# Performance work log

Measured on AMD Instinct MI355X. Metric: run time of the kernel, lower is better.

## Reference

```python
import jax, jax.numpy as jnp
import numpy as np
import math

B, N, DEG, C, F0, NCLS = 128, 512, 8, 128, 128, 10
E = B * N * DEG
RATIO = 0.8
K1 = math.ceil(RATIO * N)    # 410
K2 = math.ceil(RATIO * K1)   # 328
K3 = math.ceil(RATIO * K2)   # 263


def setup_inputs() -> dict:
    key = jax.random.key(0)
    ks = jax.random.split(key, 32)
    x = jax.random.normal(ks[0], (B * N, F0), jnp.float32)
    epg = N * DEG
    src_l = jax.random.randint(ks[1], (B, epg), 0, N)
    dst_l = jax.random.randint(ks[2], (B, epg), 0, N)
    off = (jnp.arange(B, dtype=jnp.int32) * N)[:, None]
    edge_src = (src_l + off).reshape(-1).astype(jnp.int32)
    edge_dst = (dst_l + off).reshape(-1).astype(jnp.int32)

    def lin(k, fi, fo):
        return jax.random.normal(k, (fi, fo), jnp.float32) / np.float32(np.sqrt(fi))

    inp = {"x": x, "edge_src": edge_src, "edge_dst": edge_dst}
    i = 3
    for s, fi in (("1", F0), ("2", C), ("3", C)):
        inp["Wroot" + s] = lin(ks[i], fi, C); i += 1
        inp["Wrel" + s] = lin(ks[i], fi, C); i += 1
        inp["brel" + s] = jnp.zeros((C,), jnp.float32)
        inp["p" + s] = jax.random.normal(ks[i], (C,), jnp.float32); i += 1
    inp["W1"] = lin(ks[i], 2 * C, 128); i += 1
    inp["b1"] = jnp.zeros((128,), jnp.float32)
    inp["W2"] = lin(ks[i], 128, 64); i += 1
    inp["b2"] = jnp.zeros((64,), jnp.float32)
    inp["W3"] = lin(ks[i], 64, NCLS); i += 1
    inp["b3"] = jnp.zeros((NCLS,), jnp.float32)
    return inp


def graph_conv(x, src, dst, emask, Wroot, Wrel, brel, num_nodes):
    # PyG GraphConv (aggr='add'): lin_rel(sum_j x_j) + lin_root(x_i)
    msg = x[src] * emask[:, None]                      # masked gather  [E, C]
    agg = jax.ops.segment_sum(msg, dst, num_segments=num_nodes)
    return agg @ Wrel + brel + x @ Wroot


def topk_pool(x, p, src, dst, emask, b, n, k):
    # score = tanh(x . p / ||p||), keep top-k nodes per graph, scale kept x by score
    score = jnp.tanh((x @ p) / jnp.linalg.norm(p))     # [b*n]
    vals, idx = jax.lax.top_k(score.reshape(b, n), k)  # [b, k]
    perm = (idx + (jnp.arange(b, dtype=idx.dtype) * n)[:, None]).reshape(-1)
    x_new = x[perm] * vals.reshape(-1, 1)
    inv = jnp.full((b * n,), -1, jnp.int32).at[perm].set(
        jnp.arange(b * k, dtype=jnp.int32))
    ns, nd = inv[src], inv[dst]
    nmask = emask * (ns >= 0) * (nd >= 0)
    return x_new, jnp.maximum(ns, 0), jnp.maximum(nd, 0), nmask


def readout(h, b, k):
    hb = h.reshape(b, k, -1)
    return jnp.concatenate([hb.max(axis=1), hb.mean(axis=1)], axis=-1)  # gmp||gap


def reference(x, edge_src, edge_dst,
              Wroot1, Wrel1, brel1, p1,
              Wroot2, Wrel2, brel2, p2,
              Wroot3, Wrel3, brel3, p3,
              W1, b1, W2, b2, W3, b3):
    emask = jnp.ones((E,), x.dtype)
    s, d = edge_src, edge_dst

    h = jax.nn.relu(graph_conv(x, s, d, emask, Wroot1, Wrel1, brel1, B * N))
    h, s, d, emask = topk_pool(h, p1, s, d, emask, B, N, K1)
    x1 = readout(h, B, K1)

    h = jax.nn.relu(graph_conv(h, s, d, emask, Wroot2, Wrel2, brel2, B * K1))
    h, s, d, emask = topk_pool(h, p2, s, d, emask, B, K1, K2)
    x2 = readout(h, B, K2)

    h = jax.nn.relu(graph_conv(h, s, d, emask, Wroot3, Wrel3, brel3, B * K2))
    h, s, d, emask = topk_pool(h, p3, s, d, emask, B, K2, K3)
    x3 = readout(h, B, K3)

    g = x1 + x2 + x3                                   # [B, 256]
    g = jax.nn.relu(g @ W1 + b1)                       # dropout is identity in eval
    g = jax.nn.relu(g @ W2 + b2)
    return jax.nn.log_softmax(g @ W3 + b3, axis=-1)    # [B, NCLS]
```

## Files before the change

kernel.cpp:

```cpp
#include <hip/hip_runtime.h>
#include <hip/hip_bf16.h>
#include <math.h>

#define B_G   128
#define N0    512
#define DEG   8
#define CCH   128
#define EPG   (N0*DEG)
#define E_TOTAL (B_G*EPG)
#define K1    410
#define K2    328
#define K3    263
#define NCLS  10

using bf16x8 = __attribute__((ext_vector_type(8))) __bf16;
using f32x4  = __attribute__((ext_vector_type(4))) float;
typedef unsigned short ushort;
typedef unsigned int uint;

__device__ __forceinline__ ushort f2b(float f) {
    uint u = __float_as_uint(f);
    u += 0x7fffu + ((u >> 16) & 1u);
    return (ushort)(u >> 16);
}
__device__ __forceinline__ float b2f(ushort h) {
    return __uint_as_float(((uint)h) << 16);
}
__device__ __forceinline__ void split2(float v, ushort& hi, ushort& lo) {
    hi = f2b(v);
    lo = f2b(v - b2f(hi));
}
__device__ __forceinline__ uint pksplit(float v) {
    ushort h, l; split2(v, h, l);
    return (uint)h | ((uint)l << 16);
}
__device__ __forceinline__ float unpk(uint u) {
    return __uint_as_float(u << 16) + __uint_as_float(u & 0xffff0000u);
}

__global__ void prep_kernel(const float* __restrict__ x0, uint* __restrict__ xp, int n4,
                            const float* __restrict__ Wrel0, const float* __restrict__ Wroot0,
                            const float* __restrict__ Wrel1, const float* __restrict__ Wroot1,
                            const float* __restrict__ Wrel2, const float* __restrict__ Wroot2,
                            ushort* __restrict__ Bph, ushort* __restrict__ Bpl) {
    int i = blockIdx.x * 256 + threadIdx.x;
    if (i < n4) {
        float4 v = ((const float4*)x0)[i];
        uint4 o;
        o.x = pksplit(v.x); o.y = pksplit(v.y); o.z = pksplit(v.z); o.w = pksplit(v.w);
        ((uint4*)xp)[i] = o;
    }
    if (i < 3 * 32768) {
        int layer = i >> 15, rem = i & 32767;
        int j = rem & 7, lane = (rem >> 3) & 63, cf = (rem >> 9) & 7, ks = rem >> 12;
        int k = ks * 32 + (lane >> 4) * 8 + j;
        int c = cf * 16 + (lane & 15);
        const float* Wrel  = layer == 0 ? Wrel0  : layer == 1 ? Wrel1  : Wrel2;
        const float* Wroot = layer == 0 ? Wroot0 : layer == 1 ? Wroot1 : Wroot2;
        float v = (k < 128) ? Wrel[k * 128 + c] : Wroot[(k - 128) * 128 + c];
        ushort hi, lo; split2(v, hi, lo);
        Bph[i] = hi; Bpl[i] = lo;
    }
}

__global__ __launch_bounds__(1024) void csr0_kernel(
        const int* __restrict__ es, const int* __restrict__ ed, int* __restrict__ mapT,
        int* __restrict__ indptr, int* __restrict__ counts, int* __restrict__ srclist) {
    int b = blockIdx.x, tid = threadIdx.x;
    __shared__ uint epk[EPG];
    __shared__ int cnt[512], pref[512], curs[512];
    if (tid < 512) { cnt[tid] = 0; mapT[b * N0 + tid] = b * N0 + tid; }
    __syncthreads();
    int base = b * EPG;
    for (int i = tid; i < EPG; i += 1024) {
        int s = es[base + i] & (N0 - 1);
        int d = ed[base + i] & (N0 - 1);
        epk[i] = (uint)s | ((uint)d << 16);
        atomicAdd(&cnt[d], 1);
    }
    __syncthreads();
    if (tid < 512) pref[tid] = cnt[tid];
    __syncthreads();
    for (int off = 1; off < 512; off <<= 1) {
        int v = (tid >= off && tid < 512) ? pref[tid - off] : 0;
        __syncthreads();
        if (tid < 512) pref[tid] += v;
        __syncthreads();
    }
    if (tid < 512) {
        int excl = tid ? pref[tid - 1] : 0;
        indptr[b * N0 + tid] = base + excl;
        counts[b * N0 + tid] = cnt[tid];
        curs[tid] = excl;
    }
    __syncthreads();
    for (int i = tid; i < EPG; i += 1024) {
        uint wv = epk[i];
        int dl = wv >> 16;
        int pos = atomicAdd(&curs[dl], 1);
        srclist[base + pos] = (int)(wv & 0xFFFFu);
    }
}

__global__ __launch_bounds__(1024) void aggregate(
        const uint* __restrict__ xp,
        const int* __restrict__ indptr, const int* __restrict__ counts,
        const int* __restrict__ srclist,
        uint* __restrict__ aggp, int n) {
    extern __shared__ float slab[];
    int b = blockIdx.x >> 2, q = blockIdx.x & 3;
    int tid = threadIdx.x;
    for (int t = tid; t < n * 8; t += 1024) {
        int nd = t >> 3, c4 = t & 7;
        uint4 u = *(const uint4*)&xp[(size_t)(b * n + nd) * CCH + q * 32 + c4 * 4];
        *(float4*)&slab[nd * 32 + c4 * 4] =
            make_float4(unpk(u.x), unpk(u.y), unpk(u.z), unpk(u.w));
    }
    __syncthreads();
    int wave = tid >> 6, lane = tid & 63;
    int gl = lane >> 3;
    int sub = lane & 7;
    int ngroups = (n + 7) >> 3;
    for (int g = wave; g < ngroups; g += 16) {
        int d = g * 8 + gl;
        bool act = d < n;
        int beg = 0, cnt = 0;
        if (act) { beg = indptr[b * n + d]; cnt = counts[b * n + d]; }
        float4 acc = make_float4(0.f, 0.f, 0.f, 0.f);
        int id_next = (cnt > 0) ? srclist[beg] : 0;
        for (int j = 0; j < cnt; j++) {
            int id = id_next;
            if (j + 1 < cnt) id_next = srclist[beg + j + 1];
            const float4 v = *(const float4*)&slab[id * 32 + sub * 4];
            acc.x += v.x; acc.y += v.y; acc.z += v.z; acc.w += v.w;
        }
        if (act) {
            uint4 o;
            o.x = pksplit(acc.x); o.y = pksplit(acc.y);
            o.z = pksplit(acc.z); o.w = pksplit(acc.w);
            *(uint4*)&aggp[(size_t)(b * n + d) * CCH + q * 32 + sub * 4] = o;
        }
    }
}

__global__ __launch_bounds__(512, 4) void transform_mfma(
        const uint* __restrict__ aggp, const uint* __restrict__ xp,
        const ushort* __restrict__ Bph, const ushort* __restrict__ Bpl,
        const float* __restrict__ brel, const float* __restrict__ pvec,
        uint* __restrict__ hp, float* __restrict__ score) {
    __shared__ ushort ldsBh[16384];
    __shared__ ushort ldsBl[16384];
    int tid = threadIdx.x;
    int wave = tid >> 6, lane = tid & 63;
    int r = lane & 15, kb = lane >> 4;
    int rows0 = blockIdx.x * 128 + wave * 16;

    f32x4 acc[8];
#pragma unroll
    for (int cf = 0; cf < 8; cf++) acc[cf] = (f32x4)(0.f);

    union U16 { uint u[4]; bf16x8 v; };

#pragma unroll
    for (int half = 0; half < 2; half++) {
        if (half) __syncthreads();
#pragma unroll
        for (int i = 0; i < 4; i++) {
            int idx = tid + i * 512;
            ((uint4*)ldsBh)[idx] = ((const uint4*)(Bph + half * 16384))[idx];
            ((uint4*)ldsBl)[idx] = ((const uint4*)(Bpl + half * 16384))[idx];
        }
        __syncthreads();
        const uint* A = half ? xp : aggp;
#pragma unroll
        for (int ks4 = 0; ks4 < 4; ks4++) {
            size_t rowbase = (size_t)(rows0 + r) * CCH + ks4 * 32 + kb * 8;
            uint4 ua = *(const uint4*)&A[rowbase];
            uint4 ub = *(const uint4*)&A[rowbase + 4];
            U16 ah, al;
            ah.u[0] = (ua.x & 0xffffu) | (ua.y << 16);
            ah.u[1] = (ua.z & 0xffffu) | (ua.w << 16);
            ah.u[2] = (ub.x & 0xffffu) | (ub.y << 16);
            ah.u[3] = (ub.z & 0xffffu) | (ub.w << 16);
            al.u[0] = (ua.x >> 16) | (ua.y & 0xffff0000u);
            al.u[1] = (ua.z >> 16) | (ua.w & 0xffff0000u);
            al.u[2] = (ub.x >> 16) | (ub.y & 0xffff0000u);
            al.u[3] = (ub.z >> 16) | (ub.w & 0xffff0000u);
#pragma unroll
            for (int cf = 0; cf < 8; cf++) {
                bf16x8 bh = *(const bf16x8*)&ldsBh[((ks4 * 8 + cf) * 64 + lane) * 8];
                bf16x8 bl = *(const bf16x8*)&ldsBl[((ks4 * 8 + cf) * 64 + lane) * 8];
                acc[cf] = __builtin_amdgcn_mfma_f32_16x16x32_bf16(ah.v, bl, acc[cf], 0, 0, 0);
                acc[cf] = __builtin_amdgcn_mfma_f32_16x16x32_bf16(al.v, bh, acc[cf], 0, 0, 0);
                acc[cf] = __builtin_amdgcn_mfma_f32_16x16x32_bf16(ah.v, bh, acc[cf], 0, 0, 0);
            }
        }
    }

    float pv[8], bb[8], q = 0.f;
#pragma unroll
    for (int cf = 0; cf < 8; cf++) {
        pv[cf] = pvec[cf * 16 + r];
        bb[cf] = brel[cf * 16 + r];
        q += pv[cf] * pv[cf];
    }
    float dots[4] = {0.f, 0.f, 0.f, 0.f};
#pragma unroll
    for (int cf = 0; cf < 8; cf++) {
#pragma unroll
        for (int reg = 0; reg < 4; reg++) {
            float v = acc[cf][reg] + bb[cf];
            v = v > 0.f ? v : 0.f;
            hp[(size_t)(rows0 + kb * 4 + reg) * CCH + cf * 16 + r] = pksplit(v);
            dots[reg] += v * pv[cf];
        }
    }
#pragma unroll
    for (int off = 1; off < 16; off <<= 1) {
        q += __shfl_xor(q, off);
#pragma unroll
        for (int reg = 0; reg < 4; reg++) dots[reg] += __shfl_xor(dots[reg], off);
    }
    if (r == 0) {
        float inv_norm = rsqrtf(q);
#pragma unroll
        for (int reg = 0; reg < 4; reg++)
            score[rows0 + kb * 4 + reg] = tanhf(dots[reg] * inv_norm);
    }
}

__global__ __launch_bounds__(512) void pool_kernel(
        const float* __restrict__ score, const uint* __restrict__ hp,
        uint* __restrict__ xp, float* __restrict__ gpart, int* __restrict__ mapT,
        const int* __restrict__ es, const int* __restrict__ ed,
        int* __restrict__ indptr, int* __restrict__ counts, int* __restrict__ srclist,
        int n, int k, int layer, int last) {
    int b = blockIdx.x >> 2, q = blockIdx.x & 3;
    int tid = threadIdx.x;
    __shared__ unsigned long long keys[512];
    __shared__ short invl[512];
    __shared__ float wmax[8][128], wsum[8][128];
    __shared__ int newmap[512];
    __shared__ uint epk[EPG];
    __shared__ int cnt[512], pref[512], curs[512];
    {
        unsigned long long key = 0ull;
        if (tid < n) {
            uint u = __float_as_uint(score[b * n + tid]);
            u = (u & 0x80000000u) ? ~u : (u | 0x80000000u);
            key = ((unsigned long long)u << 32) | (uint)(~tid);
        }
        keys[tid] = key;
        invl[tid] = -1;
    }
    __syncthreads();
    for (int kk2 = 2; kk2 <= 512; kk2 <<= 1) {
        for (int j = kk2 >> 1; j > 0; j >>= 1) {
            int s = tid, sxj = s ^ j;
            if (sxj > s) {
                unsigned long long a = keys[s], c = keys[sxj];
                bool doSwap = ((s & kk2) == 0) ? (a < c) : (a > c);
                if (doSwap) { keys[s] = c; keys[sxj] = a; }
            }
            __syncthreads();
        }
    }
    if (tid < k) {
        int node = (int)(~(uint)keys[tid]);
        invl[node] = (short)tid;
    }
    __syncthreads();

    if (q == 0) {
        if (last) return;
        int m = mapT[b * N0 + tid];
        int res = -1;
        if (m >= 0) {
            int nl = invl[m - b * n];
            if (nl >= 0) res = b * k + nl;
        }
        mapT[b * N0 + tid] = res;
        newmap[tid] = res;
        cnt[tid] = 0;
        __syncthreads();
        int base = b * EPG;
        int nb = b * k;
        for (int i = tid; i < EPG; i += 512) {
            int s = es[base + i] & (N0 - 1);
            int d = ed[base + i] & (N0 - 1);
            int sg = newmap[s], dg = newmap[d];
            uint wv = 0xFFFFFFFFu;
            if ((sg | dg) >= 0) {
                int sl = sg - nb, dl = dg - nb;
                wv = (uint)sl | ((uint)dl << 16);
                atomicAdd(&cnt[dl], 1);
            }
            epk[i] = wv;
        }
        __syncthreads();
        pref[tid] = cnt[tid];
        __syncthreads();
        for (int off = 1; off < 512; off <<= 1) {
            int v = (tid >= off) ? pref[tid - off] : 0;
            __syncthreads();
            pref[tid] += v;
            __syncthreads();
        }
        int excl = tid ? pref[tid - 1] : 0;
        if (tid < k) {
            indptr[nb + tid] = base + excl;
            counts[nb + tid] = cnt[tid];
        }
        curs[tid] = excl;
        __syncthreads();
        for (int i = tid; i < EPG; i += 512) {
            uint wv = epk[i];
            if (wv != 0xFFFFFFFFu) {
                int dl = wv >> 16;
                int pos = atomicAdd(&curs[dl], 1);
                srclist[base + pos] = (int)(wv & 0xFFFFu);
            }
        }
    } else {
        int p = q - 1;
        int wave = tid >> 6, lane = tid & 63;
        float mx0 = -1e30f, mx1 = -1e30f, sm0 = 0.f, sm1 = 0.f;
        for (int j = p + 3 * wave; j < k; j += 24) {
            unsigned long long key = keys[j];
            int node = (int)(~(uint)key);
            uint tu = (uint)(key >> 32);
            uint su = (tu & 0x80000000u) ? (tu & 0x7fffffffu) : ~tu;
            float v = __uint_as_float(su);
            uint2 u = ((const uint2*)(hp + (size_t)(b * n + node) * CCH))[lane];
            float c0 = unpk(u.x) * v;
            float c1 = unpk(u.y) * v;
            ((uint2*)(xp + (size_t)(b * k + j) * CCH))[lane] =
                make_uint2(pksplit(c0), pksplit(c1));
            mx0 = fmaxf(mx0, c0); sm0 += c0;
            mx1 = fmaxf(mx1, c1); sm1 += c1;
        }
        wmax[wave][2 * lane] = mx0; wmax[wave][2 * lane + 1] = mx1;
        wsum[wave][2 * lane] = sm0; wsum[wave][2 * lane + 1] = sm1;
        __syncthreads();
        if (tid < 128) {
            float m = wmax[0][tid], s = wsum[0][tid];
#pragma unroll
            for (int w = 1; w < 8; w++) { m = fmaxf(m, wmax[w][tid]); s += wsum[w][tid]; }
            float* gp = gpart + ((size_t)(layer * 3 + p) * B_G + b) * 256;
            gp[tid] = m;
            gp[128 + tid] = s;
        }
    }
}

__global__ __launch_bounds__(128) void mlp_kernel(const float* __restrict__ gpart,
        const float* __restrict__ W1, const float* __restrict__ b1,
        const float* __restrict__ W2, const float* __restrict__ b2,
        const float* __restrict__ W3, const float* __restrict__ b3,
        float* __restrict__ out) {
    int b = blockIdx.x, t = threadIdx.x;
    __shared__ float gs[256], h1[128], h2[64], lg[10];
    const float kdiv[3] = {(float)K1, (float)K2, (float)K3};
    float a0 = 0.f, a1 = 0.f;
#pragma unroll
    for (int l = 0; l < 3; l++) {
        float m = -1e30f, s = 0.f;
#pragma unroll
        for (int p = 0; p < 3; p++) {
            const float* gp = gpart + ((size_t)(l * 3 + p) * B_G + b) * 256;
            m = fmaxf(m, gp[t]);
            s += gp[128 + t];
        }
        a0 += m;
        a1 += s / kdiv[l];
    }
    gs[t] = a0;
    gs[128 + t] = a1;
    __syncthreads();
    {
        float a = b1[t];
        for (int c = 0; c < 256; c++) a += gs[c] * W1[c * 128 + t];
        h1[t] = fmaxf(a, 0.f);
    }
    __syncthreads();
    if (t < 64) {
        float a = b2[t];
        for (int c = 0; c < 128; c++) a += h1[c] * W2[c * 64 + t];
        h2[t] = fmaxf(a, 0.f);
    }
    __syncthreads();
    if (t < 10) {
        float a = b3[t];
        for (int c = 0; c < 64; c++) a += h2[c] * W3[c * 10 + t];
        lg[t] = a;
    }
    __syncthreads();
    if (t < 10) {
        float m = lg[0];
        for (int i = 1; i < 10; i++) m = fmaxf(m, lg[i]);
        float s = 0.f;
        for (int i = 0; i < 10; i++) s += expf(lg[i] - m);
        out[b * 10 + t] = lg[t] - m - logf(s);
    }
}

extern "C" void kernel_launch(void* const* d_in, const int* in_sizes, int n_in,
                              void* d_out, int out_size, void* d_ws, size_t ws_size,
                              hipStream_t stream) {
    (void)in_sizes; (void)n_in; (void)out_size; (void)ws_size;
    const float* x0 = (const float*)d_in[0];
    const int* es = (const int*)d_in[1];
    const int* ed = (const int*)d_in[2];
    const float* Wroot[3] = {(const float*)d_in[3], (const float*)d_in[7], (const float*)d_in[11]};
    const float* Wrel[3]  = {(const float*)d_in[4], (const float*)d_in[8], (const float*)d_in[12]};
    const float* brel[3]  = {(const float*)d_in[5], (const float*)d_in[9], (const float*)d_in[13]};
    const float* pvec[3]  = {(const float*)d_in[6], (const float*)d_in[10], (const float*)d_in[14]};
    const float* W1 = (const float*)d_in[15];
    const float* b1 = (const float*)d_in[16];
    const float* W2 = (const float*)d_in[17];
    const float* b2 = (const float*)d_in[18];
    const float* W3 = (const float*)d_in[19];
    const float* b3 = (const float*)d_in[20];

    size_t off = 0;
    char* base = (char*)d_ws;
    auto alloc = [&](size_t bytes) -> void* {
        void* p = base + off;
        off += (bytes + 255) & ~(size_t)255;
        return p;
    };
    const size_t FEATP = (size_t)(B_G * N0) * CCH * 4;
    uint* xp   = (uint*)alloc(FEATP);
    uint* aggp = (uint*)alloc(FEATP);
    ushort* Bph = (ushort*)alloc((size_t)3 * 32768 * 2);
    ushort* Bpl = (ushort*)alloc((size_t)3 * 32768 * 2);
    int* mapT   = (int*)alloc((size_t)(B_G * N0) * 4);
    int* counts = (int*)alloc((size_t)(B_G * N0) * 4);
    int* indptr = (int*)alloc((size_t)(B_G * N0) * 4);
    int* srclist = (int*)alloc((size_t)E_TOTAL * 4);
    float* score = (float*)alloc((size_t)(B_G * N0) * 4);
    float* gpart = (float*)alloc((size_t)3 * 3 * B_G * 256 * 4);

    const int N4 = B_G * N0 * CCH / 4;
    prep_kernel<<<(N4 + 255) / 256, 256, 0, stream>>>(
        x0, xp, N4, Wrel[0], Wroot[0], Wrel[1], Wroot[1], Wrel[2], Wroot[2], Bph, Bpl);
    csr0_kernel<<<B_G, 1024, 0, stream>>>(es, ed, mapT, indptr, counts, srclist);

    int nper[4] = {N0, K1, K2, K3};
    for (int l = 0; l < 3; l++) {
        int n = nper[l], k = nper[l + 1];
        int n_nodes = B_G * n;
        aggregate<<<4 * B_G, 1024, (size_t)n * 32 * 4, stream>>>(
            xp, indptr, counts, srclist, aggp, n);
        transform_mfma<<<n_nodes / 128, 512, 0, stream>>>(
            aggp, xp, Bph + (size_t)l * 32768, Bpl + (size_t)l * 32768,
            brel[l], pvec[l], aggp, score);
        pool_kernel<<<4 * B_G, 512, 0, stream>>>(
            score, aggp, xp, gpart, mapT, es, ed, indptr, counts, srclist,
            n, k, l, l == 2);
    }
    mlp_kernel<<<B_G, 128, 0, stream>>>(gpart, W1, b1, W2, b2, W3, b3, (float*)d_out);
}
```

Measured before the change: 219.5 us.

## Defer pooled gather via perm indices and filter CSR incrementally

Pool no longer writes the gathered, score-scaled features. It emits a perm/score list, and the next aggregate and transform gather rows through perm and apply the scale on the fly. CSR rebuilding now filters the previous per-node source lists through the inverse map, replacing the full re-scan of the original edge list. Source indices shrink to 16-bit, and the prep and CSR-setup kernels are merged into one launch. The intent is less global write traffic and fewer launches, at the cost of indirect row reads and per-thread serial edge loops in pool.

Measured after the change: 203.2 us. -7.4%, faster.

```diff
diff --git a/kernel.cpp b/kernel.cpp
--- a/kernel.cpp
+++ b/kernel.cpp
@@ -38,83 +38,86 @@
     return __uint_as_float(u << 16) + __uint_as_float(u & 0xffff0000u);
 }
 
-__global__ void prep_kernel(const float* __restrict__ x0, uint* __restrict__ xp, int n4,
-                            const float* __restrict__ Wrel0, const float* __restrict__ Wroot0,
-                            const float* __restrict__ Wrel1, const float* __restrict__ Wroot1,
-                            const float* __restrict__ Wrel2, const float* __restrict__ Wroot2,
-                            ushort* __restrict__ Bph, ushort* __restrict__ Bpl) {
-    int i = blockIdx.x * 256 + threadIdx.x;
-    if (i < n4) {
-        float4 v = ((const float4*)x0)[i];
-        uint4 o;
-        o.x = pksplit(v.x); o.y = pksplit(v.y); o.z = pksplit(v.z); o.w = pksplit(v.w);
-        ((uint4*)xp)[i] = o;
-    }
-    if (i < 3 * 32768) {
-        int layer = i >> 15, rem = i & 32767;
-        int j = rem & 7, lane = (rem >> 3) & 63, cf = (rem >> 9) & 7, ks = rem >> 12;
-        int k = ks * 32 + (lane >> 4) * 8 + j;
-        int c = cf * 16 + (lane & 15);
-        const float* Wrel  = layer == 0 ? Wrel0  : layer == 1 ? Wrel1  : Wrel2;
-        const float* Wroot = layer == 0 ? Wroot0 : layer == 1 ? Wroot1 : Wroot2;
-        float v = (k < 128) ? Wrel[k * 128 + c] : Wroot[(k - 128) * 128 + c];
-        ushort hi, lo; split2(v, hi, lo);
-        Bph[i] = hi; Bpl[i] = lo;
-    }
-}
-
-__global__ __launch_bounds__(1024) void csr0_kernel(
-        const int* __restrict__ es, const int* __restrict__ ed, int* __restrict__ mapT,
-        int* __restrict__ indptr, int* __restrict__ counts, int* __restrict__ srclist) {
-    int b = blockIdx.x, tid = threadIdx.x;
+__global__ __launch_bounds__(512) void setup_kernel(
+        const float* __restrict__ x0, uint* __restrict__ xp, int n4,
+        const float* __restrict__ Wrel0, const float* __restrict__ Wroot0,
+        const float* __restrict__ Wrel1, const float* __restrict__ Wroot1,
+        const float* __restrict__ Wrel2, const float* __restrict__ Wroot2,
+        ushort* __restrict__ Bph, ushort* __restrict__ Bpl,
+        const int* __restrict__ es, const int* __restrict__ ed,
+        int* __restrict__ indptr0, int* __restrict__ counts0, ushort* __restrict__ srclist0) {
     __shared__ uint epk[EPG];
     __shared__ int cnt[512], pref[512], curs[512];
-    if (tid < 512) { cnt[tid] = 0; mapT[b * N0 + tid] = b * N0 + tid; }
-    __syncthreads();
-    int base = b * EPG;
-    for (int i = tid; i < EPG; i += 1024) {
-        int s = es[base + i] & (N0 - 1);
-        int d = ed[base + i] & (N0 - 1);
-        epk[i] = (uint)s | ((uint)d << 16);
-        atomicAdd(&cnt[d], 1);
-    }
-    __syncthreads();
-    if (tid < 512) pref[tid] = cnt[tid];
-    __syncthreads();
-    for (int off = 1; off < 512; off <<= 1) {
-        int v = (tid >= off && tid < 512) ? pref[tid - off] : 0;
-        __syncthreads();
-        if (tid < 512) pref[tid] += v;
-        __syncthreads();
-    }
-    if (tid < 512) {
+    if (blockIdx.x < B_G) {
+        int b = blockIdx.x, tid = threadIdx.x;
+        cnt[tid] = 0;
+        __syncthreads();
+        int base = b * EPG;
+        for (int i = tid; i < EPG; i += 512) {
+            int s = es[base + i] & (N0 - 1);
+            int d = ed[base + i] & (N0 - 1);
+            epk[i] = (uint)s | ((uint)d << 16);
+            atomicAdd(&cnt[d], 1);
+        }
+        __syncthreads();
+        pref[tid] = cnt[tid];
+        __syncthreads();
+        for (int off = 1; off < 512; off <<= 1) {
+            int v = (tid >= off) ? pref[tid - off] : 0;
+            __syncthreads();
+            pref[tid] += v;
+            __syncthreads();
+        }
         int excl = tid ? pref[tid - 1] : 0;
-        indptr[b * N0 + tid] = base + excl;
-        counts[b * N0 + tid] = cnt[tid];
+        indptr0[b * N0 + tid] = base + excl;
+        counts0[b * N0 + tid] = cnt[tid];
         curs[tid] = excl;
-    }
-    __syncthreads();
-    for (int i = tid; i < EPG; i += 1024) {
-        uint wv = epk[i];
-        int dl = wv >> 16;
-        int pos = atomicAdd(&curs[dl], 1);
-        srclist[base + pos] = (int)(wv & 0xFFFFu);
+        __syncthreads();
+        for (int i = tid; i < EPG; i += 512) {
+            uint wv = epk[i];
+            int dl = wv >> 16;
+            int pos = atomicAdd(&curs[dl], 1);
+            srclist0[base + pos] = (ushort)(wv & 0xFFFFu);
+        }
+    } else {
+        int i = (blockIdx.x - B_G) * 512 + threadIdx.x;
+        if (i < n4) {
+            float4 v = ((const float4*)x0)[i];
+            uint4 o;
+            o.x = pksplit(v.x); o.y = pksplit(v.y); o.z = pksplit(v.z); o.w = pksplit(v.w);
+            ((uint4*)xp)[i] = o;
+        }
+        if (i < 3 * 32768) {
+            int layer = i >> 15, rem = i & 32767;
+            int j = rem & 7, lane = (rem >> 3) & 63, cf = (rem >> 9) & 7, ks = rem >> 12;
+            int k = ks * 32 + (lane >> 4) * 8 + j;
+            int c = cf * 16 + (lane & 15);
+            const float* Wrel  = layer == 0 ? Wrel0  : layer == 1 ? Wrel1  : Wrel2;
+            const float* Wroot = layer == 0 ? Wroot0 : layer == 1 ? Wroot1 : Wroot2;
+            float v = (k < 128) ? Wrel[k * 128 + c] : Wroot[(k - 128) * 128 + c];
+            ushort hi, lo; split2(v, hi, lo);
+            Bph[i] = hi; Bpl[i] = lo;
+        }
     }
 }
 
 __global__ __launch_bounds__(1024) void aggregate(
-        const uint* __restrict__ xp,
+        const uint* __restrict__ hin, const int* __restrict__ perm,
+        const float* __restrict__ pval,
         const int* __restrict__ indptr, const int* __restrict__ counts,
-        const int* __restrict__ srclist,
+        const ushort* __restrict__ srclist,
         uint* __restrict__ aggp, int n) {
     extern __shared__ float slab[];
     int b = blockIdx.x >> 2, q = blockIdx.x & 3;
     int tid = threadIdx.x;
     for (int t = tid; t < n * 8; t += 1024) {
         int nd = t >> 3, c4 = t & 7;
-        uint4 u = *(const uint4*)&xp[(size_t)(b * n + nd) * CCH + q * 32 + c4 * 4];
+        int gid = b * n + nd;
+        size_t old = perm ? (size_t)perm[gid] : (size_t)gid;
+        float v = perm ? pval[gid] : 1.f;
+        uint4 u = *(const uint4*)&hin[old * CCH + q * 32 + c4 * 4];
         *(float4*)&slab[nd * 32 + c4 * 4] =
-            make_float4(unpk(u.x), unpk(u.y), unpk(u.z), unpk(u.w));
+            make_float4(unpk(u.x) * v, unpk(u.y) * v, unpk(u.z) * v, unpk(u.w) * v);
     }
     __syncthreads();
     int wave = tid >> 6, lane = tid & 63;
@@ -127,10 +130,10 @@
         int beg = 0, cnt = 0;
         if (act) { beg = indptr[b * n + d]; cnt = counts[b * n + d]; }
         float4 acc = make_float4(0.f, 0.f, 0.f, 0.f);
-        int id_next = (cnt > 0) ? srclist[beg] : 0;
+        int id_next = (cnt > 0) ? (int)srclist[beg] : 0;
         for (int j = 0; j < cnt; j++) {
             int id = id_next;
-            if (j + 1 < cnt) id_next = srclist[beg + j + 1];
+            if (j + 1 < cnt) id_next = (int)srclist[beg + j + 1];
             const float4 v = *(const float4*)&slab[id * 32 + sub * 4];
             acc.x += v.x; acc.y += v.y; acc.z += v.z; acc.w += v.w;
         }
@@ -144,16 +147,20 @@
 }
 
 __global__ __launch_bounds__(512, 4) void transform_mfma(
-        const uint* __restrict__ aggp, const uint* __restrict__ xp,
+        const uint* __restrict__ aggp, const uint* __restrict__ hin,
+        const int* __restrict__ perm, const float* __restrict__ pval,
         const ushort* __restrict__ Bph, const ushort* __restrict__ Bpl,
         const float* __restrict__ brel, const float* __restrict__ pvec,
-        uint* __restrict__ hp, float* __restrict__ score) {
+        uint* __restrict__ hout, float* __restrict__ score) {
     __shared__ ushort ldsBh[16384];
     __shared__ ushort ldsBl[16384];
     int tid = threadIdx.x;
     int wave = tid >> 6, lane = tid & 63;
     int r = lane & 15, kb = lane >> 4;
     int rows0 = blockIdx.x * 128 + wave * 16;
+    int gid = rows0 + r;
+    size_t oldrow = perm ? (size_t)perm[gid] : (size_t)gid;
+    float rv = perm ? pval[gid] : 1.f;
 
     f32x4 acc[8];
 #pragma unroll
@@ -171,21 +178,36 @@
             ((uint4*)ldsBl)[idx] = ((const uint4*)(Bpl + half * 16384))[idx];
         }
         __syncthreads();
-        const uint* A = half ? xp : aggp;
+        const uint* A = half ? hin : aggp;
+        size_t abase = half ? oldrow * CCH : (size_t)gid * CCH;
 #pragma unroll
         for (int ks4 = 0; ks4 < 4; ks4++) {
-            size_t rowbase = (size_t)(rows0 + r) * CCH + ks4 * 32 + kb * 8;
+            size_t rowbase = abase + ks4 * 32 + kb * 8;
             uint4 ua = *(const uint4*)&A[rowbase];
             uint4 ub = *(const uint4*)&A[rowbase + 4];
             U16 ah, al;
-            ah.u[0] = (ua.x & 0xffffu) | (ua.y << 16);
-            ah.u[1] = (ua.z & 0xffffu) | (ua.w << 16);
-            ah.u[2] = (ub.x & 0xffffu) | (ub.y << 16);
-            ah.u[3] = (ub.z & 0xffffu) | (ub.w << 16);
-            al.u[0] = (ua.x >> 16) | (ua.y & 0xffff0000u);
-            al.u[1] = (ua.z >> 16) | (ua.w & 0xffff0000u);
-            al.u[2] = (ub.x >> 16) | (ub.y & 0xffff0000u);
-            al.u[3] = (ub.z >> 16) | (ub.w & 0xffff0000u);
+            if (half && perm) {
+                float c[8] = {unpk(ua.x) * rv, unpk(ua.y) * rv, unpk(ua.z) * rv,
+                              unpk(ua.w) * rv, unpk(ub.x) * rv, unpk(ub.y) * rv,
+                              unpk(ub.z) * rv, unpk(ub.w) * rv};
+#pragma unroll
+                for (int p2 = 0; p2 < 4; p2++) {
+                    ushort h0, l0, h1, l1;
+                    split2(c[2 * p2], h0, l0);
+                    split2(c[2 * p2 + 1], h1, l1);
+                    ah.u[p2] = (uint)h0 | ((uint)h1 << 16);
+                    al.u[p2] = (uint)l0 | ((uint)l1 << 16);
+                }
+            } else {
+                ah.u[0] = (ua.x & 0xffffu) | (ua.y << 16);
+                ah.u[1] = (ua.z & 0xffffu) | (ua.w << 16);
+                ah.u[2] = (ub.x & 0xffffu) | (ub.y << 16);
+                ah.u[3] = (ub.z & 0xffffu) | (ub.w << 16);
+                al.u[0] = (ua.x >> 16) | (ua.y & 0xffff0000u);
+                al.u[1] = (ua.z >> 16) | (ua.w & 0xffff0000u);
+                al.u[2] = (ub.x >> 16) | (ub.y & 0xffff0000u);
+                al.u[3] = (ub.z >> 16) | (ub.w & 0xffff0000u);
+            }
 #pragma unroll
             for (int cf = 0; cf < 8; cf++) {
                 bf16x8 bh = *(const bf16x8*)&ldsBh[((ks4 * 8 + cf) * 64 + lane) * 8];
@@ -211,7 +233,7 @@
         for (int reg = 0; reg < 4; reg++) {
             float v = acc[cf][reg] + bb[cf];
             v = v > 0.f ? v : 0.f;
-            hp[(size_t)(rows0 + kb * 4 + reg) * CCH + cf * 16 + r] = pksplit(v);
+            hout[(size_t)(rows0 + kb * 4 + reg) * CCH + cf * 16 + r] = pksplit(v);
             dots[reg] += v * pv[cf];
         }
     }
@@ -231,18 +253,19 @@
 
 __global__ __launch_bounds__(512) void pool_kernel(
         const float* __restrict__ score, const uint* __restrict__ hp,
-        uint* __restrict__ xp, float* __restrict__ gpart, int* __restrict__ mapT,
-        const int* __restrict__ es, const int* __restrict__ ed,
-        int* __restrict__ indptr, int* __restrict__ counts, int* __restrict__ srclist,
+        int* __restrict__ perm_out, float* __restrict__ pval_out,
+        float* __restrict__ gpart,
+        const int* __restrict__ indptr_in, const int* __restrict__ counts_in,
+        const ushort* __restrict__ srclist_in,
+        int* __restrict__ indptr_out, int* __restrict__ counts_out,
+        ushort* __restrict__ srclist_out,
         int n, int k, int layer, int last) {
     int b = blockIdx.x >> 2, q = blockIdx.x & 3;
     int tid = threadIdx.x;
     __shared__ unsigned long long keys[512];
     __shared__ short invl[512];
     __shared__ float wmax[8][128], wsum[8][128];
-    __shared__ int newmap[512];
-    __shared__ uint epk[EPG];
-    __shared__ int cnt[512], pref[512], curs[512];
+    __shared__ int cnt[512], pref[512];
     {
         unsigned long long key = 0ull;
         if (tid < n) {
@@ -273,30 +296,20 @@
 
     if (q == 0) {
         if (last) return;
-        int m = mapT[b * N0 + tid];
-        int res = -1;
-        if (m >= 0) {
-            int nl = invl[m - b * n];
-            if (nl >= 0) res = b * k + nl;
-        }
-        mapT[b * N0 + tid] = res;
-        newmap[tid] = res;
-        cnt[tid] = 0;
-        __syncthreads();
-        int base = b * EPG;
-        int nb = b * k;
-        for (int i = tid; i < EPG; i += 512) {
-            int s = es[base + i] & (N0 - 1);
-            int d = ed[base + i] & (N0 - 1);
-            int sg = newmap[s], dg = newmap[d];
-            uint wv = 0xFFFFFFFFu;
-            if ((sg | dg) >= 0) {
-                int sl = sg - nb, dl = dg - nb;
-                wv = (uint)sl | ((uint)dl << 16);
-                atomicAdd(&cnt[dl], 1);
-            }
-            epk[i] = wv;
-        }
+        int node = -1, beg = 0, c = 0, nk = 0;
+        if (tid < k) {
+            unsigned long long key = keys[tid];
+            node = (int)(~(uint)key);
+            uint tu = (uint)(key >> 32);
+            uint su = (tu & 0x80000000u) ? (tu & 0x7fffffffu) : ~tu;
+            perm_out[b * k + tid] = b * n + node;
+            pval_out[b * k + tid] = __uint_as_float(su);
+            beg = indptr_in[b * n + node];
+            c = counts_in[b * n + node];
+            for (int t = 0; t < c; t++)
+                if (invl[srclist_in[beg + t]] >= 0) nk++;
+        }
+        cnt[tid] = (tid < k) ? nk : 0;
         __syncthreads();
         pref[tid] = cnt[tid];
         __syncthreads();
@@ -306,19 +319,14 @@
             pref[tid] += v;
             __syncthreads();
         }
-        int excl = tid ? pref[tid - 1] : 0;
         if (tid < k) {
-            indptr[nb + tid] = base + excl;
-            counts[nb + tid] = cnt[tid];
-        }
-        curs[tid] = excl;
-        __syncthreads();
-        for (int i = tid; i < EPG; i += 512) {
-            uint wv = epk[i];
-            if (wv != 0xFFFFFFFFu) {
-                int dl = wv >> 16;
-                int pos = atomicAdd(&curs[dl], 1);
-                srclist[base + pos] = (int)(wv & 0xFFFFu);
+            int excl = tid ? pref[tid - 1] : 0;
+            indptr_out[b * k + tid] = b * EPG + excl;
+            counts_out[b * k + tid] = nk;
+            int pos = b * EPG + excl;
+            for (int t = 0; t < c; t++) {
+                int ns = invl[srclist_in[beg + t]];
+                if (ns >= 0) srclist_out[pos++] = (ushort)ns;
             }
         }
     } else {
@@ -334,8 +342,6 @@
             uint2 u = ((const uint2*)(hp + (size_t)(b * n + node) * CCH))[lane];
             float c0 = unpk(u.x) * v;
             float c1 = unpk(u.y) * v;
-            ((uint2*)(xp + (size_t)(b * k + j) * CCH))[lane] =
-                make_uint2(pksplit(c0), pksplit(c1));
             mx0 = fmaxf(mx0, c0); sm0 += c0;
             mx1 = fmaxf(mx1, c1); sm1 += c1;
         }
@@ -430,34 +436,52 @@
         return p;
     };
     const size_t FEATP = (size_t)(B_G * N0) * CCH * 4;
-    uint* xp   = (uint*)alloc(FEATP);
-    uint* aggp = (uint*)alloc(FEATP);
+    uint* P0 = (uint*)alloc(FEATP);
+    uint* P1 = (uint*)alloc(FEATP);
+    uint* P2 = (uint*)alloc(FEATP);
     ushort* Bph = (ushort*)alloc((size_t)3 * 32768 * 2);
     ushort* Bpl = (ushort*)alloc((size_t)3 * 32768 * 2);
-    int* mapT   = (int*)alloc((size_t)(B_G * N0) * 4);
-    int* counts = (int*)alloc((size_t)(B_G * N0) * 4);
-    int* indptr = (int*)alloc((size_t)(B_G * N0) * 4);
-    int* srclist = (int*)alloc((size_t)E_TOTAL * 4);
+    int* iptA = (int*)alloc((size_t)(B_G * N0) * 4);
+    int* cntA = (int*)alloc((size_t)(B_G * N0) * 4);
+    ushort* srcA = (ushort*)alloc((size_t)E_TOTAL * 2);
+    int* iptB = (int*)alloc((size_t)(B_G * N0) * 4);
+    int* cntB = (int*)alloc((size_t)(B_G * N0) * 4);
+    ushort* srcB = (ushort*)alloc((size_t)E_TOTAL * 2);
+    int* permA = (int*)alloc((size_t)(B_G * K1) * 4);
+    float* pvalA = (float*)alloc((size_t)(B_G * K1) * 4);
+    int* permB = (int*)alloc((size_t)(B_G * K1) * 4);
+    float* pvalB = (float*)alloc((size_t)(B_G * K1) * 4);
     float* score = (float*)alloc((size_t)(B_G * N0) * 4);
     float* gpart = (float*)alloc((size_t)3 * 3 * B_G * 256 * 4);
 
     const int N4 = B_G * N0 * CCH / 4;
-    prep_kernel<<<(N4 + 255) / 256, 256, 0, stream>>>(
-        x0, xp, N4, Wrel[0], Wroot[0], Wrel[1], Wroot[1], Wrel[2], Wroot[2], Bph, Bpl);
-    csr0_kernel<<<B_G, 1024, 0, stream>>>(es, ed, mapT, indptr, counts, srclist);
-
-    int nper[4] = {N0, K1, K2, K3};
-    for (int l = 0; l < 3; l++) {
-        int n = nper[l], k = nper[l + 1];
-        int n_nodes = B_G * n;
-        aggregate<<<4 * B_G, 1024, (size_t)n * 32 * 4, stream>>>(
-            xp, indptr, counts, srclist, aggp, n);
-        transform_mfma<<<n_nodes / 128, 512, 0, stream>>>(
-            aggp, xp, Bph + (size_t)l * 32768, Bpl + (size_t)l * 32768,
-            brel[l], pvec[l], aggp, score);
-        pool_kernel<<<4 * B_G, 512, 0, stream>>>(
-            score, aggp, xp, gpart, mapT, es, ed, indptr, counts, srclist,
-            n, k, l, l == 2);
-    }
+    setup_kernel<<<B_G + (N4 + 511) / 512, 512, 0, stream>>>(
+        x0, P2, N4, Wrel[0], Wroot[0], Wrel[1], Wroot[1], Wrel[2], Wroot[2],
+        Bph, Bpl, es, ed, iptA, cntA, srcA);
+
+    aggregate<<<4 * B_G, 1024, (size_t)N0 * 32 * 4, stream>>>(
+        P2, nullptr, nullptr, iptA, cntA, srcA, P1, N0);
+    transform_mfma<<<B_G * N0 / 128, 512, 0, stream>>>(
+        P1, P2, nullptr, nullptr, Bph, Bpl, brel[0], pvec[0], P0, score);
+    pool_kernel<<<4 * B_G, 512, 0, stream>>>(
+        score, P0, permA, pvalA, gpart, iptA, cntA, srcA, iptB, cntB, srcB,
+        N0, K1, 0, 0);
+
+    aggregate<<<4 * B_G, 1024, (size_t)K1 * 32 * 4, stream>>>(
+        P0, permA, pvalA, iptB, cntB, srcB, P1, K1);
+    transform_mfma<<<B_G * K1 / 128, 512, 0, stream>>>(
+        P1, P0, permA, pvalA, Bph + 32768, Bpl + 32768, brel[1], pvec[1], P2, score);
+    pool_kernel<<<4 * B_G, 512, 0, stream>>>(
+        score, P2, permB, pvalB, gpart, iptB, cntB, srcB, iptA, cntA, srcA,
+        K1, K2, 1, 0);
+
+    aggregate<<<4 * B_G, 1024, (size_t)K2 * 32 * 4, stream>>>(
+        P2, permB, pvalB, iptA, cntA, srcA, P1, K2);
+    transform_mfma<<<B_G * K2 / 128, 512, 0, stream>>>(
+        P1, P2, permB, pvalB, Bph + 2 * 32768, Bpl + 2 * 32768, brel[2], pvec[2], P0, score);
+    pool_kernel<<<4 * B_G, 512, 0, stream>>>(
+        score, P0, nullptr, nullptr, gpart, iptA, cntA, srcA, iptB, cntB, srcB,
+        K2, K3, 2, 1);
+
     mlp_kernel<<<B_G, 128, 0, stream>>>(gpart, W1, b1, W2, b2, W3, b3, (float*)d_out);
 }
```
